# Optimization experiments

Measured on AMD Instinct MI355X. Metric: run time of the kernel, lower is better.

The kernel has to match this reference:

```python
import jax, jax.numpy as jnp
import numpy as np

NUM_HEADS = 16
HIDDEN = 1024
HEAD_DIM = HIDDEN // NUM_HEADS
B, L = 2, 2048


def setup_inputs() -> dict:
    key = jax.random.key(0)
    ks = jax.random.split(key, 5)
    scale = 1.0 / np.sqrt(HIDDEN)
    return {
        "x": jax.random.normal(ks[0], (B, L, HIDDEN), dtype=jnp.float32),
        "Wq": jax.random.normal(ks[1], (HIDDEN, HIDDEN), dtype=jnp.float32) * scale,
        "Wk": jax.random.normal(ks[2], (HIDDEN, HIDDEN), dtype=jnp.float32) * scale,
        "Wv": jax.random.normal(ks[3], (HIDDEN, HIDDEN), dtype=jnp.float32) * scale,
        "Wo": jax.random.normal(ks[4], (HIDDEN, HIDDEN), dtype=jnp.float32) * scale,
    }


def reference(x, Wq, Wk, Wv, Wo):
    b, l, _ = x.shape
    # projections (torch nn.Linear: y = x @ W.T), reshape to (B,L,H,D)
    q = (x @ Wq.T).reshape(b, l, NUM_HEADS, HEAD_DIM)
    k = (x @ Wk.T).reshape(b, l, NUM_HEADS, HEAD_DIM)
    v = (x @ Wv.T).reshape(b, l, NUM_HEADS, HEAD_DIM)
    # positive feature map
    q = jax.nn.elu(q) + 1.0
    k = jax.nn.elu(k) + 1.0
    # causal linear attention via cumulative kv outer products
    kv = jnp.einsum('blhd,blhe->blhde', k, v)          # (B,L,H,D,D)
    kv_cumsum = jnp.cumsum(kv, axis=1)
    k_cumsum = jnp.cumsum(k, axis=1)
    out = jnp.einsum('blhd,blhde->blhe', q, kv_cumsum)  # (B,L,H,D)
    normalizer = jnp.clip(jnp.einsum('blhd,blhd->blh', q, k_cumsum), 1e-6, None)
    out = out / normalizer[..., None]
    out = out.reshape(b, l, HIDDEN)
    return out @ Wo.T
```

## Files before the change

### kernel.cpp

```cpp
#include <hip/hip_runtime.h>
#include <cstdint>
#include <cstddef>

#define HID 1024
#define NH 16
#define HD 64
#define BB 2
#define LL 2048
#define MM (BB*LL)
#define CHUNK 64
#define NT (LL/CHUNK)
#define BHn (BB*NH)

typedef __bf16 bf16;
typedef __attribute__((ext_vector_type(8))) __bf16 bf16x8;
typedef __attribute__((ext_vector_type(4))) float f32x4;

__device__ __forceinline__ f32x4 mfma16(bf16x8 a, bf16x8 b, f32x4 c){
  return __builtin_amdgcn_mfma_f32_16x16x32_bf16(a, b, c, 0, 0, 0);
}

__device__ __forceinline__ void gload16(const void* g, void* l){
  __builtin_amdgcn_global_load_lds(
      (const __attribute__((address_space(1))) unsigned int*)g,
      (__attribute__((address_space(3))) unsigned int*)l, 16, 0, 0);
}

__device__ __forceinline__ void barx(){
  asm volatile("" ::: "memory");
  __builtin_amdgcn_s_barrier();
  asm volatile("" ::: "memory");
}

#define WAITVM(N) asm volatile("s_waitcnt vmcnt(" #N ")" ::: "memory")

__global__ __launch_bounds__(256) void cast_all_k(
    const float* __restrict__ x,  const float* __restrict__ w0,
    const float* __restrict__ w1, const float* __restrict__ w2, const float* __restrict__ w3,
    bf16* __restrict__ xb, bf16* __restrict__ d0, bf16* __restrict__ d1,
    bf16* __restrict__ d2, bf16* __restrict__ d3)
{
  int bid = blockIdx.x;
  const float* s; bf16* d; int base;
  if (bid < 4096){ s = x; d = xb; base = bid; }
  else {
    int w = (bid - 4096) >> 10, r = (bid - 4096) & 1023;
    s = (w==0)?w0:(w==1)?w1:(w==2)?w2:w3;
    d = (w==0)?d0:(w==1)?d1:(w==2)?d2:d3;
    base = r;
  }
  int i = base*256 + threadIdx.x;
  float4 v = ((const float4*)s)[i];
  union { bf16 h[4]; uint2 u; } pk;
  pk.h[0]=(bf16)v.x; pk.h[1]=(bf16)v.y; pk.h[2]=(bf16)v.z; pk.h[3]=(bf16)v.w;
  *((uint2*)(d + 4*(size_t)i)) = pk.u;
}

template<int MODE>
__global__ __launch_bounds__(512, 2) void gemm8_k(
    const bf16* __restrict__ A,
    const bf16* __restrict__ W0, const bf16* __restrict__ W1, const bf16* __restrict__ W2,
    bf16* __restrict__ Qo, bf16* __restrict__ Kn, bf16* __restrict__ Vn,
    float* __restrict__ Outf)
{
  constexpr int BM  = (MODE==0) ? 256 : 128;
  constexpr int BN  = (MODE==0) ? 256 : 128;
  constexpr int AP  = BM/128;
  constexpr int BP  = BN/128;
  constexpr int PPT = AP + BP;
  constexpr int NA  = BM/32;
  constexpr int NBF = BN/64;
  constexpr int NKT = HID/32;
  __shared__ bf16 lds[4][PPT][128*32];

  const int tid = threadIdx.x;
  const int wv = tid >> 6, lane = tid & 63;
  const int lrow = lane & 15, g4 = lane >> 4;
  const int wr = wv >> 2, wc = wv & 3;
  int bn = blockIdx.x, wsel = 0;
  const bf16* W = W0;
  if (MODE==0){ wsel = bn >> 2; bn &= 3; W = (wsel==0)?W0:((wsel==1)?W1:W2); }
  const int row0 = blockIdx.y*BM, col0 = bn*BN;

  const int sr = tid >> 2, sc = tid & 3;
  const int scs = sc ^ ((sr>>1)&3);
  const bf16* gA0 = A + (size_t)(row0 + sr)*HID + scs*8;
  const bf16* gA1 = gA0 + (size_t)128*HID;
  const bf16* gB0 = W + (size_t)(col0 + sr)*HID + scs*8;
  const bf16* gB1 = gB0 + (size_t)128*HID;
  const int ldst = tid*8;

  auto stage_tile = [&](int u){
    const int buf = u & 3;
    gload16(gA0 + u*32, (void*)&lds[buf][0][ldst]);
    if constexpr (AP==2) gload16(gA1 + u*32, (void*)&lds[buf][1][ldst]);
    gload16(gB0 + u*32, (void*)&lds[buf][AP][ldst]);
    if constexpr (BP==2) gload16(gB1 + u*32, (void*)&lds[buf][AP+1][ldst]);
  };

  const int koff = (g4 ^ ((lrow>>1)&3)) << 3;

  auto read_frags = [&](int u, bf16x8 (&fa)[NA], bf16x8 (&fb)[NBF]){
    const int buf = u & 3;
    #pragma unroll
    for (int i=0;i<NA;i++){
      if constexpr (MODE==0)
        fa[i] = *(const bf16x8*)&lds[buf][wr][((i*16+lrow)<<5) + koff];
      else
        fa[i] = *(const bf16x8*)&lds[buf][0][((wr*64 + i*16+lrow)<<5) + koff];
    }
    #pragma unroll
    for (int j=0;j<NBF;j++){
      if constexpr (MODE==0)
        fb[j] = *(const bf16x8*)&lds[buf][2+(wc>>1)][(((wc&1)*64 + j*16+lrow)<<5) + koff];
      else
        fb[j] = *(const bf16x8*)&lds[buf][1][((wc*32 + j*16+lrow)<<5) + koff];
    }
  };

  f32x4 acc[NA][NBF] = {};
  auto do_mfma = [&](bf16x8 (&fa)[NA], bf16x8 (&fb)[NBF]){
    __builtin_amdgcn_s_setprio(1);
    #pragma unroll
    for (int i=0;i<NA;i++)
      #pragma unroll
      for (int j=0;j<NBF;j++)
        acc[i][j] = mfma16(fa[i], fb[j], acc[i][j]);
    __builtin_amdgcn_s_setprio(0);
  };

  stage_tile(0); stage_tile(1); stage_tile(2);
  if constexpr (MODE==0) WAITVM(8); else WAITVM(4);
  barx();
  bf16x8 fEa[NA], fEb[NBF], fOa[NA], fOb[NBF];
  read_frags(0, fEa, fEb);

  for (int t=0; t<NKT; t+=2){
    if (t+3 < NKT)      { stage_tile(t+3); if constexpr (MODE==0) WAITVM(8); else WAITVM(4); }
    else if (t+3 == NKT){ if constexpr (MODE==0) WAITVM(4); else WAITVM(2); }
    else                { WAITVM(0); }
    barx();
    read_frags(t+1, fOa, fOb);
    do_mfma(fEa, fEb);
    const int t2 = t+1;
    if (t2 < NKT-1){
      if (t2+3 < NKT)      { stage_tile(t2+3); if constexpr (MODE==0) WAITVM(8); else WAITVM(4); }
      else if (t2+3 == NKT){ if constexpr (MODE==0) WAITVM(4); else WAITVM(2); }
      else                 { WAITVM(0); }
      barx();
      read_frags(t2+1, fEa, fEb);
    }
    do_mfma(fOa, fOb);
  }

  #pragma unroll
  for (int i=0;i<NA;i++){
    const int m0 = row0 + wr*(BM/2) + i*16 + g4*4;
    #pragma unroll
    for (int j=0;j<NBF;j++){
      const int c = col0 + wc*(BN/4) + j*16 + lrow;
      #pragma unroll
      for (int r=0;r<4;r++){
        float v = acc[i][j][r];
        if (MODE==1){
          Outf[(size_t)(m0+r)*HID + c] = v;
        } else {
          if (wsel<2) v = v>0.f ? v+1.f : __expf(v);
          bf16 bv = (bf16)v;
          if      (wsel==0) Qo[(size_t)(m0+r)*HID + c] = bv;
          else if (wsel==1) Kn[(size_t)(m0+r)*HID + c] = bv;
          else              Vn[(size_t)(m0+r)*HID + c] = bv;
        }
      }
    }
  }
}

__global__ __launch_bounds__(256) void trans_k(const bf16* __restrict__ Kn, const bf16* __restrict__ Vn,
                                               bf16* __restrict__ Kt, bf16* __restrict__ Vt){
  __shared__ bf16 T[64][72];
  const bf16* src = blockIdx.z ? Vn : Kn;
  bf16* dst = blockIdx.z ? Vt : Kt;
  const int bh = blockIdx.y;
  const int b = bh >> 4, h = bh & 15;
  const int l0 = blockIdx.x * 64;
  const int t = threadIdx.x;
  const int lr = t >> 2, c4 = t & 3;
  const bf16* s = src + ((size_t)(b*LL + l0 + lr))*HID + h*HD;
  *(bf16x8*)&T[lr][c4*8]      = *(const bf16x8*)&s[c4*8];
  *(bf16x8*)&T[lr][c4*8 + 32] = *(const bf16x8*)&s[c4*8 + 32];
  __syncthreads();
  bf16* dd = dst + ((size_t)bh*HD + lr)*LL + l0;
  bf16x8 o0, o1;
  #pragma unroll
  for (int e=0;e<8;e++){ o0[e] = T[c4*8+e][lr]; o1[e] = T[c4*8+32+e][lr]; }
  *(bf16x8*)&dd[c4*8] = o0;
  *(bf16x8*)&dd[c4*8+32] = o1;
}

__global__ __launch_bounds__(64) void pass1_k(const bf16* __restrict__ Kt, const bf16* __restrict__ Vt,
                                              float* __restrict__ SkvT, float* __restrict__ ksum)
{
  const int blk = blockIdx.x;
  const int bh = blk >> 5, t = blk & (NT-1);
  const int lane = threadIdx.x;
  const int lrow = lane&15, g4 = lane>>4, lk8 = g4*8;
  const bf16* vtb = Vt + (size_t)bh*HD*LL + t*CHUNK;
  const bf16* ktb = Kt + (size_t)bh*HD*LL + t*CHUNK;
  bf16x8 av[4][2], bk[4][2];
  #pragma unroll
  for (int i=0;i<4;i++)
    #pragma unroll
    for (int kk=0;kk<2;kk++){
      av[i][kk] = *(const bf16x8*)&vtb[(size_t)(i*16+lrow)*LL + kk*32 + lk8];
      bk[i][kk] = *(const bf16x8*)&ktb[(size_t)(i*16+lrow)*LL + kk*32 + lk8];
    }
  f32x4 acc[4][4] = {};
  #pragma unroll
  for (int i=0;i<4;i++)
    #pragma unroll
    for (int j=0;j<4;j++)
      #pragma unroll
      for (int kk=0;kk<2;kk++)
        acc[i][j] = mfma16(av[i][kk], bk[j][kk], acc[i][j]);
  float* so = SkvT + (size_t)blk*4096;
  #pragma unroll
  for (int i=0;i<4;i++)
    #pragma unroll
    for (int j=0;j<4;j++)
      #pragma unroll
      for (int r=0;r<4;r++)
        so[(i*16+g4*4+r)*64 + j*16+lrow] = acc[i][j][r];
  const bf16* krow = ktb + (size_t)lane*LL;
  float s = 0.f;
  #pragma unroll
  for (int c8=0;c8<8;c8++){
    bf16x8 v = *(const bf16x8*)&krow[c8*8];
    #pragma unroll
    for (int j=0;j<8;j++) s += (float)v[j];
  }
  ksum[(size_t)blk*64 + lane] = s;
}

__global__ __launch_bounds__(256) void pass2_k(const float* __restrict__ SkvT, const float* __restrict__ ksum,
                                               bf16* __restrict__ Sexcl, float* __restrict__ ksx)
{
  int gid = blockIdx.x*256 + threadIdx.x;
  if (gid < BHn*4096){
    int bh = gid >> 12, e = gid & 4095;
    float run = 0.f;
    size_t base = (size_t)bh*NT*4096 + e;
    for (int t=0;t<NT;t++){
      Sexcl[base + (size_t)t*4096] = (bf16)run;
      run += SkvT[base + (size_t)t*4096];
    }
  } else if (gid < BHn*4096 + BHn*64){
    int g2 = gid - BHn*4096;
    int bh = g2 >> 6, d = g2 & 63;
    float run = 0.f;
    size_t base = (size_t)bh*NT*64 + d;
    for (int t=0;t<NT;t++){
      ksx[base + (size_t)t*64] = run;
      run += ksum[base + (size_t)t*64];
    }
  }
}

__global__ __launch_bounds__(64) void pass3_k(const bf16* __restrict__ Q, const bf16* __restrict__ Kn,
                                              const bf16* __restrict__ Sexcl, const bf16* __restrict__ Vt,
                                              const float* __restrict__ ksx, bf16* __restrict__ Obuf)
{
  __shared__ bf16 P[64*72];
  const int blk = blockIdx.x;
  const int bh = blk>>5, t = blk&(NT-1);
  const int b = bh>>4, h = bh&15;
  const int lane = threadIdx.x;
  const int lrow = lane&15, g4 = lane>>4, lk8 = g4*8;
  const bf16* qb = Q  + ((size_t)(b*LL + t*CHUNK))*HID + h*HD;
  const bf16* kb = Kn + ((size_t)(b*LL + t*CHUNK))*HID + h*HD;
  bf16x8 aq[4][2], bk[4][2];
  #pragma unroll
  for (int i=0;i<4;i++)
    #pragma unroll
    for (int kk=0;kk<2;kk++){
      aq[i][kk] = *(const bf16x8*)&qb[(size_t)(i*16+lrow)*HID + kk*32 + lk8];
      bk[i][kk] = *(const bf16x8*)&kb[(size_t)(i*16+lrow)*HID + kk*32 + lk8];
    }
  f32x4 sacc[4][4] = {};
  #pragma unroll
  for (int i=0;i<4;i++)
    #pragma unroll
    for (int j=0;j<4;j++)
      #pragma unroll
      for (int kk=0;kk<2;kk++)
        sacc[i][j] = mfma16(aq[i][kk], bk[j][kk], sacc[i][j]);
  float rs[4][4];
  #pragma unroll
  for (int i=0;i<4;i++)
    #pragma unroll
    for (int r=0;r<4;r++){
      int irow = i*16 + g4*4 + r;
      float p = 0.f;
      #pragma unroll
      for (int j=0;j<4;j++){
        int jcol = j*16 + lrow;
        float v = (jcol <= irow) ? sacc[i][j][r] : 0.f;
        sacc[i][j][r] = v;
        p += v;
      }
      p += __shfl_xor(p,1); p += __shfl_xor(p,2);
      p += __shfl_xor(p,4); p += __shfl_xor(p,8);
      rs[i][r] = p;
    }
  #pragma unroll
  for (int i=0;i<4;i++)
    #pragma unroll
    for (int j=0;j<4;j++)
      #pragma unroll
      for (int r=0;r<4;r++)
        P[(i*16+g4*4+r)*72 + j*16+lrow] = (bf16)sacc[i][j][r];
  const float* kp = ksx + (size_t)blk*64;
  float zA[4];
  #pragma unroll
  for (int i=0;i<4;i++){
    float s = 0.f;
    #pragma unroll
    for (int kk=0;kk<2;kk++){
      const float* k8 = kp + kk*32 + lk8;
      bf16x8 q = aq[i][kk];
      #pragma unroll
      for (int j=0;j<8;j++) s += (float)q[j] * k8[j];
    }
    s += __shfl_xor(s,16); s += __shfl_xor(s,32);
    zA[i] = s;
  }
  const bf16* sb = Sexcl + (size_t)blk*4096;
  f32x4 oacc[4][4] = {};
  bf16x8 bs[4][2];
  #pragma unroll
  for (int j=0;j<4;j++)
    #pragma unroll
    for (int kk=0;kk<2;kk++)
      bs[j][kk] = *(const bf16x8*)&sb[(size_t)(j*16+lrow)*64 + kk*32 + lk8];
  #pragma unroll
  for (int i=0;i<4;i++)
    #pragma unroll
    for (int j=0;j<4;j++)
      #pragma unroll
      for (int kk=0;kk<2;kk++)
        oacc[i][j] = mfma16(aq[i][kk], bs[j][kk], oacc[i][j]);
  __syncthreads();
  const bf16* vb = Vt + (size_t)bh*HD*LL + t*CHUNK;
  bf16x8 bv[4][2], ap[4][2];
  #pragma unroll
  for (int j=0;j<4;j++)
    #pragma unroll
    for (int kk=0;kk<2;kk++)
      bv[j][kk] = *(const bf16x8*)&vb[(size_t)(j*16+lrow)*LL + kk*32 + lk8];
  #pragma unroll
  for (int i=0;i<4;i++)
    #pragma unroll
    for (int kk=0;kk<2;kk++)
      ap[i][kk] = *(const bf16x8*)&P[(i*16+lrow)*72 + kk*32 + lk8];
  #pragma unroll
  for (int i=0;i<4;i++)
    #pragma unroll
    for (int j=0;j<4;j++)
      #pragma unroll
      for (int kk=0;kk<2;kk++)
        oacc[i][j] = mfma16(ap[i][kk], bv[j][kk], oacc[i][j]);
  bf16* ob = Obuf + ((size_t)(b*LL + t*CHUNK))*HID + h*HD;
  #pragma unroll
  for (int i=0;i<4;i++)
    #pragma unroll
    for (int r=0;r<4;r++){
      float z = __shfl(zA[i], g4*4 + r) + rs[i][r];
      z = fmaxf(z, 1e-6f);
      float inv = 1.0f/z;
      int irow = i*16 + g4*4 + r;
      #pragma unroll
      for (int j=0;j<4;j++)
        ob[(size_t)irow*HID + j*16+lrow] = (bf16)(oacc[i][j][r]*inv);
    }
}

extern "C" void kernel_launch(void* const* d_in, const int* in_sizes, int n_in,
                              void* d_out, int out_size, void* d_ws, size_t ws_size,
                              hipStream_t stream)
{
  const float* x  = (const float*)d_in[0];
  const float* Wq = (const float*)d_in[1];
  const float* Wk = (const float*)d_in[2];
  const float* Wv = (const float*)d_in[3];
  const float* Wo = (const float*)d_in[4];
  float* out = (float*)d_out;

  char* p = (char*)d_ws;
  auto alloc = [&](size_t bytes){ void* r = (void*)p; p += (bytes + 255) & ~(size_t)255; return r; };
  bf16* xb   = (bf16*)alloc((size_t)MM*HID*2);
  bf16* Wqb  = (bf16*)alloc((size_t)HID*HID*2);
  bf16* Wkb  = (bf16*)alloc((size_t)HID*HID*2);
  bf16* Wvb  = (bf16*)alloc((size_t)HID*HID*2);
  bf16* Wob  = (bf16*)alloc((size_t)HID*HID*2);
  bf16* Qb   = (bf16*)alloc((size_t)MM*HID*2);
  bf16* Knb  = (bf16*)alloc((size_t)MM*HID*2);
  bf16* Vnb  = (bf16*)alloc((size_t)MM*HID*2);
  bf16* Ktb  = (bf16*)alloc((size_t)MM*HID*2);
  bf16* Vtb  = (bf16*)alloc((size_t)MM*HID*2);
  bf16* Ob   = (bf16*)alloc((size_t)MM*HID*2);
  float* SkvT  = (float*)alloc((size_t)BHn*NT*4096*4);
  bf16*  Sexcl = (bf16*) alloc((size_t)BHn*NT*4096*2);
  float* ksum  = (float*)alloc((size_t)BHn*NT*64*4);
  float* ksx   = (float*)alloc((size_t)BHn*NT*64*4);

  cast_all_k<<<dim3(8192), 256, 0, stream>>>(x, Wq,Wk,Wv,Wo, xb, Wqb,Wkb,Wvb,Wob);
  gemm8_k<0><<<dim3(12,16), 512, 0, stream>>>(xb, Wqb,Wkb,Wvb, Qb,Knb,Vnb, nullptr);
  trans_k<<<dim3(LL/64, BHn, 2), 256, 0, stream>>>(Knb, Vnb, Ktb, Vtb);
  pass1_k<<<dim3(BHn*NT), 64, 0, stream>>>(Ktb, Vtb, SkvT, ksum);
  pass2_k<<<dim3((BHn*4096 + BHn*64 + 255)/256), 256, 0, stream>>>(SkvT, ksum, Sexcl, ksx);
  pass3_k<<<dim3(BHn*NT), 64, 0, stream>>>(Qb, Knb, Sexcl, Vtb, ksx, Ob);
  gemm8_k<1><<<dim3(8,32), 512, 0, stream>>>(Ob, Wob,nullptr,nullptr, nullptr,nullptr,nullptr, out);
}
```

Before: 171.9 us.

## Fuse transpose, chunk state and prefix scan into one sequential per-head scan kernel

Replaces the transpose, per-chunk KV outer-product and separate prefix-scan kernels with a single kernel per (batch, head). It walks the chunks in order, transposing K/V in double-buffered shared memory and accumulating the running state in MFMA registers, and writes the exclusive prefix state directly. pass3 now transposes V in shared memory itself instead of reading a pre-transposed copy. This removes two launches and the fp32 intermediate round-trips, but the scan runs only 32 blocks with a serial loop over 32 chunks, which leaves most of the GPU idle during that phase.

```diff
diff --git a/kernel.cpp b/kernel.cpp
--- a/kernel.cpp
+++ b/kernel.cpp
@@ -176,108 +176,110 @@
   }
 }
 
-__global__ __launch_bounds__(256) void trans_k(const bf16* __restrict__ Kn, const bf16* __restrict__ Vn,
-                                               bf16* __restrict__ Kt, bf16* __restrict__ Vt){
-  __shared__ bf16 T[64][72];
-  const bf16* src = blockIdx.z ? Vn : Kn;
-  bf16* dst = blockIdx.z ? Vt : Kt;
-  const int bh = blockIdx.y;
-  const int b = bh >> 4, h = bh & 15;
-  const int l0 = blockIdx.x * 64;
-  const int t = threadIdx.x;
-  const int lr = t >> 2, c4 = t & 3;
-  const bf16* s = src + ((size_t)(b*LL + l0 + lr))*HID + h*HD;
-  *(bf16x8*)&T[lr][c4*8]      = *(const bf16x8*)&s[c4*8];
-  *(bf16x8*)&T[lr][c4*8 + 32] = *(const bf16x8*)&s[c4*8 + 32];
+#define SPAD 78
+__global__ __launch_bounds__(256) void scan_k(const bf16* __restrict__ Kn, const bf16* __restrict__ Vn,
+                                              bf16* __restrict__ Sexcl, float* __restrict__ ksx)
+{
+  __shared__ bf16 KT[2][64*SPAD];
+  __shared__ bf16 VT[2][64*SPAD];
+  const int bh = blockIdx.x;
+  const int b = bh>>4, h = bh&15;
+  const int tid = threadIdx.x;
+  const int wv = tid>>6, lane = tid&63;
+  const int lrow = lane&15, g4 = lane>>4, lk8 = g4*8;
+  const int we = wv>>1, wd = wv&1;
+  const int sj = tid>>2, c4 = tid&3;
+  const bf16* kbase = Kn + ((size_t)b*LL)*HID + h*HD;
+  const bf16* vbase = Vn + ((size_t)b*LL)*HID + h*HD;
+
+  bf16x8 kr0, kr1, vr0, vr1;
+  auto gload = [&](int t){
+    const bf16* ks = kbase + (size_t)(t*CHUNK + sj)*HID + c4*16;
+    const bf16* vs = vbase + (size_t)(t*CHUNK + sj)*HID + c4*16;
+    kr0 = *(const bf16x8*)&ks[0]; kr1 = *(const bf16x8*)&ks[8];
+    vr0 = *(const bf16x8*)&vs[0]; vr1 = *(const bf16x8*)&vs[8];
+  };
+  auto lwrite = [&](int buf){
+    #pragma unroll
+    for (int e=0;e<8;e++){
+      KT[buf][(c4*16+e)*SPAD + sj]   = kr0[e];
+      KT[buf][(c4*16+8+e)*SPAD + sj] = kr1[e];
+      VT[buf][(c4*16+e)*SPAD + sj]   = vr0[e];
+      VT[buf][(c4*16+8+e)*SPAD + sj] = vr1[e];
+    }
+  };
+
+  f32x4 S[2][2] = {};
+  float kv = 0.f;
+  gload(0); lwrite(0);
   __syncthreads();
-  bf16* dd = dst + ((size_t)bh*HD + lr)*LL + l0;
-  bf16x8 o0, o1;
-  #pragma unroll
-  for (int e=0;e<8;e++){ o0[e] = T[c4*8+e][lr]; o1[e] = T[c4*8+32+e][lr]; }
-  *(bf16x8*)&dd[c4*8] = o0;
-  *(bf16x8*)&dd[c4*8+32] = o1;
-}
-
-__global__ __launch_bounds__(64) void pass1_k(const bf16* __restrict__ Kt, const bf16* __restrict__ Vt,
-                                              float* __restrict__ SkvT, float* __restrict__ ksum)
-{
-  const int blk = blockIdx.x;
-  const int bh = blk >> 5, t = blk & (NT-1);
-  const int lane = threadIdx.x;
-  const int lrow = lane&15, g4 = lane>>4, lk8 = g4*8;
-  const bf16* vtb = Vt + (size_t)bh*HD*LL + t*CHUNK;
-  const bf16* ktb = Kt + (size_t)bh*HD*LL + t*CHUNK;
-  bf16x8 av[4][2], bk[4][2];
-  #pragma unroll
-  for (int i=0;i<4;i++)
+
+  for (int t=0; t<NT; ++t){
+    const int buf = t & 1;
+    if (t+1 < NT) gload(t+1);
+    bf16* so = Sexcl + ((size_t)bh*NT + t)*4096;
+    #pragma unroll
+    for (int i=0;i<2;i++)
+      #pragma unroll
+      for (int j2=0;j2<2;j2++)
+        #pragma unroll
+        for (int r=0;r<4;r++)
+          so[(we*32 + i*16 + g4*4 + r)*64 + wd*32 + j2*16 + lrow] = (bf16)S[i][j2][r];
+    if (wv==0){
+      ksx[((size_t)bh*NT + t)*64 + lane] = kv;
+      float s = 0.f;
+      #pragma unroll
+      for (int c8=0;c8<8;c8++){
+        bf16x8 k8 = *(const bf16x8*)&KT[buf][lane*SPAD + c8*8];
+        #pragma unroll
+        for (int u=0;u<8;u++) s += (float)k8[u];
+      }
+      kv += s;
+    }
+    bf16x8 fa[2], fb[2];
     #pragma unroll
     for (int kk=0;kk<2;kk++){
-      av[i][kk] = *(const bf16x8*)&vtb[(size_t)(i*16+lrow)*LL + kk*32 + lk8];
-      bk[i][kk] = *(const bf16x8*)&ktb[(size_t)(i*16+lrow)*LL + kk*32 + lk8];
-    }
-  f32x4 acc[4][4] = {};
-  #pragma unroll
-  for (int i=0;i<4;i++)
-    #pragma unroll
-    for (int j=0;j<4;j++)
-      #pragma unroll
-      for (int kk=0;kk<2;kk++)
-        acc[i][j] = mfma16(av[i][kk], bk[j][kk], acc[i][j]);
-  float* so = SkvT + (size_t)blk*4096;
-  #pragma unroll
-  for (int i=0;i<4;i++)
-    #pragma unroll
-    for (int j=0;j<4;j++)
-      #pragma unroll
-      for (int r=0;r<4;r++)
-        so[(i*16+g4*4+r)*64 + j*16+lrow] = acc[i][j][r];
-  const bf16* krow = ktb + (size_t)lane*LL;
-  float s = 0.f;
-  #pragma unroll
-  for (int c8=0;c8<8;c8++){
-    bf16x8 v = *(const bf16x8*)&krow[c8*8];
-    #pragma unroll
-    for (int j=0;j<8;j++) s += (float)v[j];
-  }
-  ksum[(size_t)blk*64 + lane] = s;
-}
-
-__global__ __launch_bounds__(256) void pass2_k(const float* __restrict__ SkvT, const float* __restrict__ ksum,
-                                               bf16* __restrict__ Sexcl, float* __restrict__ ksx)
-{
-  int gid = blockIdx.x*256 + threadIdx.x;
-  if (gid < BHn*4096){
-    int bh = gid >> 12, e = gid & 4095;
-    float run = 0.f;
-    size_t base = (size_t)bh*NT*4096 + e;
-    for (int t=0;t<NT;t++){
-      Sexcl[base + (size_t)t*4096] = (bf16)run;
-      run += SkvT[base + (size_t)t*4096];
-    }
-  } else if (gid < BHn*4096 + BHn*64){
-    int g2 = gid - BHn*4096;
-    int bh = g2 >> 6, d = g2 & 63;
-    float run = 0.f;
-    size_t base = (size_t)bh*NT*64 + d;
-    for (int t=0;t<NT;t++){
-      ksx[base + (size_t)t*64] = run;
-      run += ksum[base + (size_t)t*64];
-    }
+      #pragma unroll
+      for (int i=0;i<2;i++)
+        fa[i] = *(const bf16x8*)&VT[buf][(we*32 + i*16 + lrow)*SPAD + kk*32 + lk8];
+      #pragma unroll
+      for (int j2=0;j2<2;j2++)
+        fb[j2] = *(const bf16x8*)&KT[buf][(wd*32 + j2*16 + lrow)*SPAD + kk*32 + lk8];
+      #pragma unroll
+      for (int i=0;i<2;i++)
+        #pragma unroll
+        for (int j2=0;j2<2;j2++)
+          S[i][j2] = mfma16(fa[i], fb[j2], S[i][j2]);
+    }
+    if (t+1 < NT) lwrite((t+1)&1);
+    __syncthreads();
   }
 }
 
 __global__ __launch_bounds__(64) void pass3_k(const bf16* __restrict__ Q, const bf16* __restrict__ Kn,
-                                              const bf16* __restrict__ Sexcl, const bf16* __restrict__ Vt,
+                                              const bf16* __restrict__ Sexcl, const bf16* __restrict__ Vn,
                                               const float* __restrict__ ksx, bf16* __restrict__ Obuf)
 {
   __shared__ bf16 P[64*72];
+  __shared__ bf16 VT[64*SPAD];
   const int blk = blockIdx.x;
   const int bh = blk>>5, t = blk&(NT-1);
   const int b = bh>>4, h = bh&15;
   const int lane = threadIdx.x;
   const int lrow = lane&15, g4 = lane>>4, lk8 = g4*8;
+  const int sj4 = lane>>2, c4 = lane&3;
   const bf16* qb = Q  + ((size_t)(b*LL + t*CHUNK))*HID + h*HD;
   const bf16* kb = Kn + ((size_t)(b*LL + t*CHUNK))*HID + h*HD;
+  const bf16* vb = Vn + ((size_t)(b*LL + t*CHUNK))*HID + h*HD;
+
+  bf16x8 vv[8];
+  #pragma unroll
+  for (int p=0;p<4;p++){
+    const bf16* vr = vb + (size_t)(p*16 + sj4)*HID + c4*16;
+    vv[p*2+0] = *(const bf16x8*)&vr[0];
+    vv[p*2+1] = *(const bf16x8*)&vr[8];
+  }
+
   bf16x8 aq[4][2], bk[4][2];
   #pragma unroll
   for (int i=0;i<4;i++)
@@ -319,6 +321,13 @@
       #pragma unroll
       for (int r=0;r<4;r++)
         P[(i*16+g4*4+r)*72 + j*16+lrow] = (bf16)sacc[i][j][r];
+  #pragma unroll
+  for (int p=0;p<4;p++)
+    #pragma unroll
+    for (int u=0;u<8;u++){
+      VT[(c4*16+u)*SPAD   + p*16 + sj4] = vv[p*2+0][u];
+      VT[(c4*16+8+u)*SPAD + p*16 + sj4] = vv[p*2+1][u];
+    }
   const float* kp = ksx + (size_t)blk*64;
   float zA[4];
   #pragma unroll
@@ -350,13 +359,12 @@
       for (int kk=0;kk<2;kk++)
         oacc[i][j] = mfma16(aq[i][kk], bs[j][kk], oacc[i][j]);
   __syncthreads();
-  const bf16* vb = Vt + (size_t)bh*HD*LL + t*CHUNK;
   bf16x8 bv[4][2], ap[4][2];
   #pragma unroll
   for (int j=0;j<4;j++)
     #pragma unroll
     for (int kk=0;kk<2;kk++)
-      bv[j][kk] = *(const bf16x8*)&vb[(size_t)(j*16+lrow)*LL + kk*32 + lk8];
+      bv[j][kk] = *(const bf16x8*)&VT[(j*16+lrow)*SPAD + kk*32 + lk8];
   #pragma unroll
   for (int i=0;i<4;i++)
     #pragma unroll
@@ -405,19 +413,13 @@
   bf16* Qb   = (bf16*)alloc((size_t)MM*HID*2);
   bf16* Knb  = (bf16*)alloc((size_t)MM*HID*2);
   bf16* Vnb  = (bf16*)alloc((size_t)MM*HID*2);
-  bf16* Ktb  = (bf16*)alloc((size_t)MM*HID*2);
-  bf16* Vtb  = (bf16*)alloc((size_t)MM*HID*2);
   bf16* Ob   = (bf16*)alloc((size_t)MM*HID*2);
-  float* SkvT  = (float*)alloc((size_t)BHn*NT*4096*4);
   bf16*  Sexcl = (bf16*) alloc((size_t)BHn*NT*4096*2);
-  float* ksum  = (float*)alloc((size_t)BHn*NT*64*4);
   float* ksx   = (float*)alloc((size_t)BHn*NT*64*4);
 
   cast_all_k<<<dim3(8192), 256, 0, stream>>>(x, Wq,Wk,Wv,Wo, xb, Wqb,Wkb,Wvb,Wob);
   gemm8_k<0><<<dim3(12,16), 512, 0, stream>>>(xb, Wqb,Wkb,Wvb, Qb,Knb,Vnb, nullptr);
-  trans_k<<<dim3(LL/64, BHn, 2), 256, 0, stream>>>(Knb, Vnb, Ktb, Vtb);
-  pass1_k<<<dim3(BHn*NT), 64, 0, stream>>>(Ktb, Vtb, SkvT, ksum);
-  pass2_k<<<dim3((BHn*4096 + BHn*64 + 255)/256), 256, 0, stream>>>(SkvT, ksum, Sexcl, ksx);
-  pass3_k<<<dim3(BHn*NT), 64, 0, stream>>>(Qb, Knb, Sexcl, Vtb, ksx, Ob);
+  scan_k<<<dim3(BHn), 256, 0, stream>>>(Knb, Vnb, Sexcl, ksx);
+  pass3_k<<<dim3(BHn*NT), 64, 0, stream>>>(Qb, Knb, Sexcl, Vnb, ksx, Ob);
   gemm8_k<1><<<dim3(8,32), 512, 0, stream>>>(Ob, Wob,nullptr,nullptr, nullptr,nullptr,nullptr, out);
 }
```

New measurement: 182.0 us. 5.9% more time.

## Fuse K/V transpose into chunk kernels and widen them to four waves

Applied to the files above, without the earlier changes.

Removes the separate transpose kernel and its Kt/Vt buffers. The chunk-state and output kernels now load K and V rows directly and transpose them in LDS. Both kernels move from one wave to four waves per block, each wave owning 16 rows, to raise parallelism and cut per-thread register use. The prefix-scan loops also get unroll pragmas. The cost is extra LDS traffic with scattered 2-byte transposed stores that may cause bank conflicts.

```diff
diff --git a/kernel.cpp b/kernel.cpp
--- a/kernel.cpp
+++ b/kernel.cpp
@@ -11,6 +11,7 @@
 #define CHUNK 64
 #define NT (LL/CHUNK)
 #define BHn (BB*NH)
+#define SP 72
 
 typedef __bf16 bf16;
 typedef __attribute__((ext_vector_type(8))) __bf16 bf16x8;
@@ -176,70 +177,65 @@
   }
 }
 
-__global__ __launch_bounds__(256) void trans_k(const bf16* __restrict__ Kn, const bf16* __restrict__ Vn,
-                                               bf16* __restrict__ Kt, bf16* __restrict__ Vt){
-  __shared__ bf16 T[64][72];
-  const bf16* src = blockIdx.z ? Vn : Kn;
-  bf16* dst = blockIdx.z ? Vt : Kt;
-  const int bh = blockIdx.y;
-  const int b = bh >> 4, h = bh & 15;
-  const int l0 = blockIdx.x * 64;
-  const int t = threadIdx.x;
-  const int lr = t >> 2, c4 = t & 3;
-  const bf16* s = src + ((size_t)(b*LL + l0 + lr))*HID + h*HD;
-  *(bf16x8*)&T[lr][c4*8]      = *(const bf16x8*)&s[c4*8];
-  *(bf16x8*)&T[lr][c4*8 + 32] = *(const bf16x8*)&s[c4*8 + 32];
-  __syncthreads();
-  bf16* dd = dst + ((size_t)bh*HD + lr)*LL + l0;
-  bf16x8 o0, o1;
-  #pragma unroll
-  for (int e=0;e<8;e++){ o0[e] = T[c4*8+e][lr]; o1[e] = T[c4*8+32+e][lr]; }
-  *(bf16x8*)&dd[c4*8] = o0;
-  *(bf16x8*)&dd[c4*8+32] = o1;
-}
-
-__global__ __launch_bounds__(64) void pass1_k(const bf16* __restrict__ Kt, const bf16* __restrict__ Vt,
-                                              float* __restrict__ SkvT, float* __restrict__ ksum)
-{
+__global__ __launch_bounds__(256) void pass1_k(const bf16* __restrict__ Kn, const bf16* __restrict__ Vn,
+                                               float* __restrict__ SkvT, float* __restrict__ ksum)
+{
+  __shared__ bf16 KT[64*SP];
+  __shared__ bf16 VT[64*SP];
   const int blk = blockIdx.x;
   const int bh = blk >> 5, t = blk & (NT-1);
-  const int lane = threadIdx.x;
+  const int b = bh>>4, h = bh&15;
+  const int tid = threadIdx.x;
+  const int we = tid >> 6, lane = tid & 63;
   const int lrow = lane&15, g4 = lane>>4, lk8 = g4*8;
-  const bf16* vtb = Vt + (size_t)bh*HD*LL + t*CHUNK;
-  const bf16* ktb = Kt + (size_t)bh*HD*LL + t*CHUNK;
-  bf16x8 av[4][2], bk[4][2];
-  #pragma unroll
-  for (int i=0;i<4;i++)
-    #pragma unroll
-    for (int kk=0;kk<2;kk++){
-      av[i][kk] = *(const bf16x8*)&vtb[(size_t)(i*16+lrow)*LL + kk*32 + lk8];
-      bk[i][kk] = *(const bf16x8*)&ktb[(size_t)(i*16+lrow)*LL + kk*32 + lk8];
-    }
-  f32x4 acc[4][4] = {};
-  #pragma unroll
-  for (int i=0;i<4;i++)
-    #pragma unroll
-    for (int j=0;j<4;j++)
+  const int sj = tid >> 2, c4 = tid & 3;
+  const bf16* kb = Kn + ((size_t)(b*LL + t*CHUNK))*HID + h*HD;
+  const bf16* vb = Vn + ((size_t)(b*LL + t*CHUNK))*HID + h*HD;
+
+  {
+    const bf16* ks = kb + (size_t)sj*HID + c4*16;
+    const bf16* vs = vb + (size_t)sj*HID + c4*16;
+    bf16x8 kr0 = *(const bf16x8*)&ks[0], kr1 = *(const bf16x8*)&ks[8];
+    bf16x8 vr0 = *(const bf16x8*)&vs[0], vr1 = *(const bf16x8*)&vs[8];
+    #pragma unroll
+    for (int e=0;e<8;e++){
+      KT[(c4*16+e)*SP + sj]   = kr0[e];
+      KT[(c4*16+8+e)*SP + sj] = kr1[e];
+      VT[(c4*16+e)*SP + sj]   = vr0[e];
+      VT[(c4*16+8+e)*SP + sj] = vr1[e];
+    }
+  }
+  __syncthreads();
+
+  f32x4 acc[4] = {};
+  #pragma unroll
+  for (int kk=0;kk<2;kk++){
+    bf16x8 fa = *(const bf16x8*)&VT[(we*16 + lrow)*SP + kk*32 + lk8];
+    #pragma unroll
+    for (int j=0;j<4;j++){
+      bf16x8 fb = *(const bf16x8*)&KT[(j*16 + lrow)*SP + kk*32 + lk8];
+      acc[j] = mfma16(fa, fb, acc[j]);
+    }
+  }
+  float* so = SkvT + (size_t)blk*4096;
+  #pragma unroll
+  for (int j=0;j<4;j++)
+    #pragma unroll
+    for (int r=0;r<4;r++)
+      so[(we*16 + g4*4 + r)*64 + j*16 + lrow] = acc[j][r];
+
+  {
+    const int row = we*16 + lrow;
+    float s = 0.f;
+    #pragma unroll
+    for (int u=0;u<2;u++){
+      bf16x8 k8 = *(const bf16x8*)&KT[row*SP + g4*16 + u*8];
       #pragma unroll
-      for (int kk=0;kk<2;kk++)
-        acc[i][j] = mfma16(av[i][kk], bk[j][kk], acc[i][j]);
-  float* so = SkvT + (size_t)blk*4096;
-  #pragma unroll
-  for (int i=0;i<4;i++)
-    #pragma unroll
-    for (int j=0;j<4;j++)
-      #pragma unroll
-      for (int r=0;r<4;r++)
-        so[(i*16+g4*4+r)*64 + j*16+lrow] = acc[i][j][r];
-  const bf16* krow = ktb + (size_t)lane*LL;
-  float s = 0.f;
-  #pragma unroll
-  for (int c8=0;c8<8;c8++){
-    bf16x8 v = *(const bf16x8*)&krow[c8*8];
-    #pragma unroll
-    for (int j=0;j<8;j++) s += (float)v[j];
-  }
-  ksum[(size_t)blk*64 + lane] = s;
+      for (int e=0;e<8;e++) s += (float)k8[e];
+    }
+    s += __shfl_xor(s,16); s += __shfl_xor(s,32);
+    if (g4==0) ksum[(size_t)blk*64 + row] = s;
+  }
 }
 
 __global__ __launch_bounds__(256) void pass2_k(const float* __restrict__ SkvT, const float* __restrict__ ksum,
@@ -250,6 +246,7 @@
     int bh = gid >> 12, e = gid & 4095;
     float run = 0.f;
     size_t base = (size_t)bh*NT*4096 + e;
+    #pragma unroll 4
     for (int t=0;t<NT;t++){
       Sexcl[base + (size_t)t*4096] = (bf16)run;
       run += SkvT[base + (size_t)t*4096];
@@ -259,6 +256,7 @@
     int bh = g2 >> 6, d = g2 & 63;
     float run = 0.f;
     size_t base = (size_t)bh*NT*64 + d;
+    #pragma unroll 4
     for (int t=0;t<NT;t++){
       ksx[base + (size_t)t*64] = run;
       run += ksum[base + (size_t)t*64];
@@ -266,122 +264,112 @@
   }
 }
 
-__global__ __launch_bounds__(64) void pass3_k(const bf16* __restrict__ Q, const bf16* __restrict__ Kn,
-                                              const bf16* __restrict__ Sexcl, const bf16* __restrict__ Vt,
-                                              const float* __restrict__ ksx, bf16* __restrict__ Obuf)
-{
-  __shared__ bf16 P[64*72];
+__global__ __launch_bounds__(256) void pass3_k(const bf16* __restrict__ Q, const bf16* __restrict__ Kn,
+                                               const bf16* __restrict__ Sexcl, const bf16* __restrict__ Vn,
+                                               const float* __restrict__ ksx, bf16* __restrict__ Obuf)
+{
+  __shared__ bf16 P[64*SP];
+  __shared__ bf16 VT[64*SP];
   const int blk = blockIdx.x;
   const int bh = blk>>5, t = blk&(NT-1);
   const int b = bh>>4, h = bh&15;
-  const int lane = threadIdx.x;
+  const int tid = threadIdx.x;
+  const int w = tid>>6, lane = tid&63;
   const int lrow = lane&15, g4 = lane>>4, lk8 = g4*8;
+  const int sj = tid>>2, c4 = tid&3;
   const bf16* qb = Q  + ((size_t)(b*LL + t*CHUNK))*HID + h*HD;
   const bf16* kb = Kn + ((size_t)(b*LL + t*CHUNK))*HID + h*HD;
-  bf16x8 aq[4][2], bk[4][2];
-  #pragma unroll
-  for (int i=0;i<4;i++)
-    #pragma unroll
-    for (int kk=0;kk<2;kk++){
-      aq[i][kk] = *(const bf16x8*)&qb[(size_t)(i*16+lrow)*HID + kk*32 + lk8];
-      bk[i][kk] = *(const bf16x8*)&kb[(size_t)(i*16+lrow)*HID + kk*32 + lk8];
-    }
-  f32x4 sacc[4][4] = {};
-  #pragma unroll
-  for (int i=0;i<4;i++)
+  const bf16* vb = Vn + ((size_t)(b*LL + t*CHUNK))*HID + h*HD;
+
+  {
+    const bf16* vs = vb + (size_t)sj*HID + c4*16;
+    bf16x8 vr0 = *(const bf16x8*)&vs[0], vr1 = *(const bf16x8*)&vs[8];
+    #pragma unroll
+    for (int e=0;e<8;e++){
+      VT[(c4*16+e)*SP + sj]   = vr0[e];
+      VT[(c4*16+8+e)*SP + sj] = vr1[e];
+    }
+  }
+
+  bf16x8 aq[2], bk[4][2];
+  #pragma unroll
+  for (int kk=0;kk<2;kk++){
+    aq[kk] = *(const bf16x8*)&qb[(size_t)(w*16+lrow)*HID + kk*32 + lk8];
     #pragma unroll
     for (int j=0;j<4;j++)
-      #pragma unroll
-      for (int kk=0;kk<2;kk++)
-        sacc[i][j] = mfma16(aq[i][kk], bk[j][kk], sacc[i][j]);
-  float rs[4][4];
-  #pragma unroll
-  for (int i=0;i<4;i++)
-    #pragma unroll
-    for (int r=0;r<4;r++){
-      int irow = i*16 + g4*4 + r;
-      float p = 0.f;
-      #pragma unroll
-      for (int j=0;j<4;j++){
-        int jcol = j*16 + lrow;
-        float v = (jcol <= irow) ? sacc[i][j][r] : 0.f;
-        sacc[i][j][r] = v;
-        p += v;
-      }
-      p += __shfl_xor(p,1); p += __shfl_xor(p,2);
-      p += __shfl_xor(p,4); p += __shfl_xor(p,8);
-      rs[i][r] = p;
-    }
-  #pragma unroll
-  for (int i=0;i<4;i++)
+      bk[j][kk] = *(const bf16x8*)&kb[(size_t)(j*16+lrow)*HID + kk*32 + lk8];
+  }
+  f32x4 sacc[4] = {};
+  #pragma unroll
+  for (int kk=0;kk<2;kk++)
     #pragma unroll
     for (int j=0;j<4;j++)
-      #pragma unroll
-      for (int r=0;r<4;r++)
-        P[(i*16+g4*4+r)*72 + j*16+lrow] = (bf16)sacc[i][j][r];
+      sacc[j] = mfma16(aq[kk], bk[j][kk], sacc[j]);
+  float rs[4];
+  #pragma unroll
+  for (int r=0;r<4;r++){
+    int irow = w*16 + g4*4 + r;
+    float p = 0.f;
+    #pragma unroll
+    for (int j=0;j<4;j++){
+      int jcol = j*16 + lrow;
+      float v = (jcol <= irow) ? sacc[j][r] : 0.f;
+      sacc[j][r] = v;
+      p += v;
+    }
+    p += __shfl_xor(p,1); p += __shfl_xor(p,2);
+    p += __shfl_xor(p,4); p += __shfl_xor(p,8);
+    rs[r] = p;
+  }
+  #pragma unroll
+  for (int j=0;j<4;j++)
+    #pragma unroll
+    for (int r=0;r<4;r++)
+      P[(w*16+g4*4+r)*SP + j*16+lrow] = (bf16)sacc[j][r];
   const float* kp = ksx + (size_t)blk*64;
-  float zA[4];
-  #pragma unroll
-  for (int i=0;i<4;i++){
+  float zA;
+  {
     float s = 0.f;
     #pragma unroll
     for (int kk=0;kk<2;kk++){
       const float* k8 = kp + kk*32 + lk8;
-      bf16x8 q = aq[i][kk];
+      bf16x8 q = aq[kk];
       #pragma unroll
       for (int j=0;j<8;j++) s += (float)q[j] * k8[j];
     }
     s += __shfl_xor(s,16); s += __shfl_xor(s,32);
-    zA[i] = s;
+    zA = s;
   }
   const bf16* sb = Sexcl + (size_t)blk*4096;
-  f32x4 oacc[4][4] = {};
-  bf16x8 bs[4][2];
-  #pragma unroll
-  for (int j=0;j<4;j++)
-    #pragma unroll
-    for (int kk=0;kk<2;kk++)
-      bs[j][kk] = *(const bf16x8*)&sb[(size_t)(j*16+lrow)*64 + kk*32 + lk8];
-  #pragma unroll
-  for (int i=0;i<4;i++)
+  f32x4 oacc[4] = {};
+  #pragma unroll
+  for (int kk=0;kk<2;kk++)
+    #pragma unroll
+    for (int j=0;j<4;j++){
+      bf16x8 bs = *(const bf16x8*)&sb[(size_t)(j*16+lrow)*64 + kk*32 + lk8];
+      oacc[j] = mfma16(aq[kk], bs, oacc[j]);
+    }
+  __syncthreads();
+  #pragma unroll
+  for (int kk=0;kk<2;kk++){
+    bf16x8 ap = *(const bf16x8*)&P[(w*16+lrow)*SP + kk*32 + lk8];
+    #pragma unroll
+    for (int j=0;j<4;j++){
+      bf16x8 bv = *(const bf16x8*)&VT[(j*16+lrow)*SP + kk*32 + lk8];
+      oacc[j] = mfma16(ap, bv, oacc[j]);
+    }
+  }
+  bf16* ob = Obuf + ((size_t)(b*LL + t*CHUNK))*HID + h*HD;
+  #pragma unroll
+  for (int r=0;r<4;r++){
+    float z = __shfl(zA, g4*4 + r) + rs[r];
+    z = fmaxf(z, 1e-6f);
+    float inv = 1.0f/z;
+    int irow = w*16 + g4*4 + r;
     #pragma unroll
     for (int j=0;j<4;j++)
-      #pragma unroll
-      for (int kk=0;kk<2;kk++)
-        oacc[i][j] = mfma16(aq[i][kk], bs[j][kk], oacc[i][j]);
-  __syncthreads();
-  const bf16* vb = Vt + (size_t)bh*HD*LL + t*CHUNK;
-  bf16x8 bv[4][2], ap[4][2];
-  #pragma unroll
-  for (int j=0;j<4;j++)
-    #pragma unroll
-    for (int kk=0;kk<2;kk++)
-      bv[j][kk] = *(const bf16x8*)&vb[(size_t)(j*16+lrow)*LL + kk*32 + lk8];
-  #pragma unroll
-  for (int i=0;i<4;i++)
-    #pragma unroll
-    for (int kk=0;kk<2;kk++)
-      ap[i][kk] = *(const bf16x8*)&P[(i*16+lrow)*72 + kk*32 + lk8];
-  #pragma unroll
-  for (int i=0;i<4;i++)
-    #pragma unroll
-    for (int j=0;j<4;j++)
-      #pragma unroll
-      for (int kk=0;kk<2;kk++)
-        oacc[i][j] = mfma16(ap[i][kk], bv[j][kk], oacc[i][j]);
-  bf16* ob = Obuf + ((size_t)(b*LL + t*CHUNK))*HID + h*HD;
-  #pragma unroll
-  for (int i=0;i<4;i++)
-    #pragma unroll
-    for (int r=0;r<4;r++){
-      float z = __shfl(zA[i], g4*4 + r) + rs[i][r];
-      z = fmaxf(z, 1e-6f);
-      float inv = 1.0f/z;
-      int irow = i*16 + g4*4 + r;
-      #pragma unroll
-      for (int j=0;j<4;j++)
-        ob[(size_t)irow*HID + j*16+lrow] = (bf16)(oacc[i][j][r]*inv);
-    }
+      ob[(size_t)irow*HID + j*16+lrow] = (bf16)(oacc[j][r]*inv);
+  }
 }
 
 extern "C" void kernel_launch(void* const* d_in, const int* in_sizes, int n_in,
@@ -405,8 +393,6 @@
   bf16* Qb   = (bf16*)alloc((size_t)MM*HID*2);
   bf16* Knb  = (bf16*)alloc((size_t)MM*HID*2);
   bf16* Vnb  = (bf16*)alloc((size_t)MM*HID*2);
-  bf16* Ktb  = (bf16*)alloc((size_t)MM*HID*2);
-  bf16* Vtb  = (bf16*)alloc((size_t)MM*HID*2);
   bf16* Ob   = (bf16*)alloc((size_t)MM*HID*2);
   float* SkvT  = (float*)alloc((size_t)BHn*NT*4096*4);
   bf16*  Sexcl = (bf16*) alloc((size_t)BHn*NT*4096*2);
@@ -415,9 +401,8 @@
 
   cast_all_k<<<dim3(8192), 256, 0, stream>>>(x, Wq,Wk,Wv,Wo, xb, Wqb,Wkb,Wvb,Wob);
   gemm8_k<0><<<dim3(12,16), 512, 0, stream>>>(xb, Wqb,Wkb,Wvb, Qb,Knb,Vnb, nullptr);
-  trans_k<<<dim3(LL/64, BHn, 2), 256, 0, stream>>>(Knb, Vnb, Ktb, Vtb);
-  pass1_k<<<dim3(BHn*NT), 64, 0, stream>>>(Ktb, Vtb, SkvT, ksum);
+  pass1_k<<<dim3(BHn*NT), 256, 0, stream>>>(Knb, Vnb, SkvT, ksum);
   pass2_k<<<dim3((BHn*4096 + BHn*64 + 255)/256), 256, 0, stream>>>(SkvT, ksum, Sexcl, ksx);
-  pass3_k<<<dim3(BHn*NT), 64, 0, stream>>>(Qb, Knb, Sexcl, Vtb, ksx, Ob);
+  pass3_k<<<dim3(BHn*NT), 256, 0, stream>>>(Qb, Knb, Sexcl, Vnb, ksx, Ob);
   gemm8_k<1><<<dim3(8,32), 512, 0, stream>>>(Ob, Wob,nullptr,nullptr, nullptr,nullptr,nullptr, out);
 }
```

New measurement: 159.1 us. 1.08x faster.
